# Kernel tuning notes

Hardware: AMD Instinct MI355X
Metric: run time of the kernel (lower is better)

The kernel has to match this reference:

```python
import jax, jax.numpy as jnp
import numpy as np

N, F_IN, H = 8192, 256, 64


def setup_inputs() -> dict:
    key = jax.random.key(0)
    ks = jax.random.split(key, 5)
    seq1 = jax.random.normal(ks[0], (1, N, F_IN), jnp.float32)
    seq2 = jax.random.normal(ks[1], (1, N, F_IN), jnp.float32)
    # dense (row-stochastic-ish) adjacency, batch dim 1 as in DGI usage
    adj = jax.random.uniform(ks[2], (1, N, N), jnp.float32) / np.float32(N)
    msk = jnp.ones((1, N), jnp.float32)
    # GCN params: Linear(in_ft, out_ft, bias=False) weight [H, F_IN], bias [H], PReLU alpha
    fc_w = jax.random.normal(ks[3], (H, F_IN), jnp.float32) / np.float32(np.sqrt(F_IN))
    gcn_bias = jnp.zeros((H,), jnp.float32)
    prelu_alpha = jnp.array(0.25, jnp.float32)
    # Discriminator: Bilinear(H, H, 1) -> weight [H, H], bias scalar
    disc_w = jax.random.normal(ks[4], (H, H), jnp.float32) / np.float32(np.sqrt(H))
    disc_b = jnp.zeros((1,), jnp.float32)
    return {"seq1": seq1, "seq2": seq2, "adj": adj, "msk": msk,
            "fc_w": fc_w, "gcn_bias": gcn_bias, "prelu_alpha": prelu_alpha,
            "disc_w": disc_w, "disc_b": disc_b}


def _gcn(seq, adj, fc_w, bias, alpha):
    fts = jnp.einsum('bnf,hf->bnh', seq, fc_w)          # linear, no bias
    out = jnp.einsum('bnm,bmh->bnh', adj, fts) + bias   # dense aggregation + bias
    return jnp.where(out > 0, out, alpha * out)          # PReLU


def reference(seq1, seq2, adj, msk, fc_w, gcn_bias, prelu_alpha, disc_w, disc_b):
    h1 = _gcn(seq1, adj, fc_w, gcn_bias, prelu_alpha)    # [1, N, H]
    # AvgReadout with mask: sum(seq*msk,1)/sum(msk)
    c = jnp.sum(h1 * msk[..., None], axis=1) / jnp.sum(msk)  # [1, H]
    c = jax.nn.sigmoid(c)
    h2 = _gcn(seq2, adj, fc_w, gcn_bias, prelu_alpha)    # [1, N, H]
    # Bilinear discriminator: sc[b,n] = h[b,n,:] @ W @ c[b,:] + b
    wc = jnp.einsum('hk,bk->bh', disc_w, c)              # [1, H]
    sc1 = jnp.einsum('bnh,bh->bn', h1, wc) + disc_b[0]   # [1, N]
    sc2 = jnp.einsum('bnh,bh->bn', h2, wc) + disc_b[0]   # [1, N]
    return jnp.concatenate([sc1, sc2], axis=1)           # [1, 2N]
```

## Files before the change

kernel.cpp:

```cpp
#include <hip/hip_runtime.h>
#include <cstdint>
#include <cstddef>

#define NN 8192
#define FIN 256
#define HH 64
#define SPLIT 16
#define KLEN (NN / SPLIT)

typedef float vf4 __attribute__((ext_vector_type(4)));
typedef short vbf8 __attribute__((ext_vector_type(8)));

__device__ inline unsigned pk_trunc(float lo, float hi) {
  return __builtin_amdgcn_perm(__float_as_uint(hi), __float_as_uint(lo), 0x07060302u);
}
__device__ inline unsigned short bf_rne(float x) {
  unsigned u = __float_as_uint(x);
  return (unsigned short)((u + 0x7FFFu + ((u >> 16) & 1u)) >> 16);
}
__device__ inline float bf_to_f(unsigned short s) {
  return __uint_as_float(((unsigned)s) << 16);
}

union FragU { unsigned u[4]; unsigned short s[8]; vbf8 v; };

__device__ inline vbf8 frag_trunc(vf4 a, vf4 b) {
  FragU t;
  t.u[0] = pk_trunc(a[0], a[1]);
  t.u[1] = pk_trunc(a[2], a[3]);
  t.u[2] = pk_trunc(b[0], b[1]);
  t.u[3] = pk_trunc(b[2], b[3]);
  return t.v;
}
__device__ inline vbf8 frag_rne(vf4 a, vf4 b) {
  FragU t;
  t.s[0] = bf_rne(a[0]); t.s[1] = bf_rne(a[1]); t.s[2] = bf_rne(a[2]); t.s[3] = bf_rne(a[3]);
  t.s[4] = bf_rne(b[0]); t.s[5] = bf_rne(b[1]); t.s[6] = bf_rne(b[2]); t.s[7] = bf_rne(b[3]);
  return t.v;
}

__device__ inline void gl_lds16(const void* g, void* l) {
  __builtin_amdgcn_global_load_lds(
      (const __attribute__((address_space(1))) void*)g,
      (__attribute__((address_space(3))) void*)l, 16, 0, 0);
}

__global__ __launch_bounds__(256) void k1_fts(
    const float* __restrict__ seq1, const float* __restrict__ seq2,
    const float* __restrict__ fcw, unsigned short* __restrict__ Bt,
    float* __restrict__ csum) {
  const int bx = blockIdx.x;
  const int s = bx & 1, mb = bx >> 1;
  const int wave = threadIdx.x >> 6, lane = threadIdx.x & 63;
  const int r = lane & 15, q = lane >> 4;
  const int m0 = mb * 64 + wave * 16;
  if (bx == 0 && threadIdx.x < 64) csum[threadIdx.x] = 0.f;
  const float* seq = s ? seq2 : seq1;
  const float* ap = seq + (size_t)(m0 + r) * FIN + q * 8;
  const float* bp = fcw + (size_t)r * FIN + q * 8;
  vf4 acc[4] = {};
#pragma unroll
  for (int kk = 0; kk < FIN; kk += 32) {
    vf4 a0 = *(const vf4*)ap;
    vf4 a1 = *(const vf4*)(ap + 4);
    vbf8 af = frag_rne(a0, a1);
#pragma unroll
    for (int f = 0; f < 4; ++f) {
      vf4 b0 = *(const vf4*)(bp + (size_t)f * 16 * FIN);
      vf4 b1 = *(const vf4*)(bp + (size_t)f * 16 * FIN + 4);
      vbf8 bfr = frag_rne(b0, b1);
      acc[f] = __builtin_amdgcn_mfma_f32_16x16x32_bf16(af, bfr, acc[f], 0, 0, 0);
    }
    ap += 32; bp += 32;
  }
#pragma unroll
  for (int f = 0; f < 4; ++f) {
    short4 v;
    v.x = (short)bf_rne(acc[f][0]);
    v.y = (short)bf_rne(acc[f][1]);
    v.z = (short)bf_rne(acc[f][2]);
    v.w = (short)bf_rne(acc[f][3]);
    unsigned short* dst = Bt + (size_t)(64 * s + 16 * f + r) * NN + m0 + q * 4;
    *(short4*)dst = v;
  }
}

__global__ __launch_bounds__(512, 4) void k2_agg(
    const float* __restrict__ adj, const unsigned short* __restrict__ Bt,
    unsigned short* __restrict__ Cpart) {
  constexpr int CHUNKS = KLEN / 128;
  __shared__ unsigned short lds[2][16384];
  const int bx = blockIdx.x;
  const int slice = bx & (SPLIT - 1), mb = bx / SPLIT;
  const int wave = threadIdx.x >> 6, lane = threadIdx.x & 63;
  const int r = lane & 15, q = lane >> 4;
  const int m0 = mb * 256 + wave * 32;
  const int k0 = slice * KLEN;

  auto stage = [&](int ch, int b) {
#pragma unroll
    for (int j = 0; j < 4; ++j) {
      const int g = j * 512 + wave * 64 + lane;
      const int r_ = g & 15, q_ = (g >> 4) & 3, f_ = (g >> 6) & 7, kk_ = g >> 9;
      const unsigned short* src =
          Bt + (size_t)(f_ * 16 + r_) * NN + k0 + ch * 128 + kk_ * 32 + q_ * 8;
      gl_lds16(src, &lds[b][(size_t)(j * 512 + wave * 64) * 8]);
    }
  };

  vf4 acc0[8] = {}, acc1[8] = {};
  const float* a_base0 = adj + (size_t)(m0 + r) * NN + k0 + q * 8;
  const float* a_base1 = a_base0 + (size_t)16 * NN;

  stage(0, 0);
#pragma unroll 1
  for (int ch = 0; ch < CHUNKS; ++ch) {
    __syncthreads();
    if (ch + 1 < CHUNKS) stage(ch + 1, (ch + 1) & 1);
    const int b = ch & 1;
#pragma unroll
    for (int kk = 0; kk < 4; ++kk) {
      const int kc = ch * 128 + kk * 32;
      vf4 a00 = __builtin_nontemporal_load((const vf4*)(a_base0 + kc));
      vf4 a01 = __builtin_nontemporal_load((const vf4*)(a_base0 + kc) + 1);
      vf4 a10 = __builtin_nontemporal_load((const vf4*)(a_base1 + kc));
      vf4 a11 = __builtin_nontemporal_load((const vf4*)(a_base1 + kc) + 1);
      vbf8 af0 = frag_trunc(a00, a01);
      vbf8 af1 = frag_trunc(a10, a11);
#pragma unroll
      for (int f = 0; f < 8; ++f) {
        vbf8 bfr = *(const vbf8*)&lds[b][(size_t)(kk * 512 + f * 64 + lane) * 8];
        acc0[f] = __builtin_amdgcn_mfma_f32_16x16x32_bf16(af0, bfr, acc0[f], 0, 0, 0);
        acc1[f] = __builtin_amdgcn_mfma_f32_16x16x32_bf16(af1, bfr, acc1[f], 0, 0, 0);
      }
    }
  }

#pragma unroll
  for (int f = 0; f < 8; ++f) {
    short4 v0, v1;
    v0.x = (short)bf_rne(acc0[f][0]); v0.y = (short)bf_rne(acc0[f][1]);
    v0.z = (short)bf_rne(acc0[f][2]); v0.w = (short)bf_rne(acc0[f][3]);
    v1.x = (short)bf_rne(acc1[f][0]); v1.y = (short)bf_rne(acc1[f][1]);
    v1.z = (short)bf_rne(acc1[f][2]); v1.w = (short)bf_rne(acc1[f][3]);
    unsigned short* d0 = Cpart + ((size_t)slice * 128 + f * 16 + r) * NN + m0 + q * 4;
    *(short4*)d0 = v0;
    *(short4*)(d0 + 16) = v1;
  }
}

__global__ __launch_bounds__(256) void k3a(
    const unsigned short* __restrict__ Cpart, const float* __restrict__ bias,
    const float* __restrict__ alpha_p, const float* __restrict__ msk,
    unsigned short* __restrict__ H, float* __restrict__ csum) {
  const int n = blockIdx.x >> 2, chunk = blockIdx.x & 3;
  const int t = threadIdx.x;
  const int m0 = chunk * 2048 + t * 8;
  const float alpha = alpha_p[0], b = bias[n & 63];
  float v[8] = {};
#pragma unroll
  for (int s = 0; s < SPLIT; ++s) {
    vbf8 c = *(const vbf8*)(Cpart + ((size_t)s * 128 + n) * NN + m0);
#pragma unroll
    for (int j = 0; j < 8; ++j) v[j] += bf_to_f((unsigned short)c[j]);
  }
  FragU hout;
  float acc = 0.f;
#pragma unroll
  for (int j = 0; j < 8; ++j) {
    float x = v[j] + b;
    x = x > 0.f ? x : alpha * x;
    hout.s[j] = bf_rne(x);
    acc += x * msk[m0 + j];
  }
  *(vbf8*)(H + (size_t)n * NN + m0) = hout.v;
  if (n < 64) {
    __shared__ float red[256];
    red[t] = acc;
    __syncthreads();
    for (int off = 128; off > 32; off >>= 1) {
      if (t < off) red[t] += red[t + off];
      __syncthreads();
    }
    if (t < 32) {
      float x = red[t] + red[t + 32];
#pragma unroll
      for (int off = 16; off > 0; off >>= 1) x += __shfl_down(x, off, 64);
      if (t == 0) atomicAdd(&csum[n], x);
    }
  }
}

__global__ __launch_bounds__(256) void k3b(
    const float* __restrict__ msk, const float* __restrict__ csum,
    const float* __restrict__ discw, float* __restrict__ wc) {
  const int t = threadIdx.x;
  __shared__ float red[256];
  __shared__ float c_sh[64];
  float ms = 0.f;
  for (int i = 0; i < 32; ++i) ms += msk[t + 256 * i];
  red[t] = ms;
  __syncthreads();
  for (int off = 128; off > 0; off >>= 1) {
    if (t < off) red[t] += red[t + off];
    __syncthreads();
  }
  if (t < 64) c_sh[t] = 1.f / (1.f + __expf(-csum[t] / red[0]));
  __syncthreads();
  if (t < 64) {
    float w = 0.f;
#pragma unroll
    for (int k = 0; k < 64; ++k) w += discw[t * 64 + k] * c_sh[k];
    wc[t] = w;
  }
}

__global__ __launch_bounds__(256) void k4_sc(
    const unsigned short* __restrict__ H, const float* __restrict__ wc,
    const float* __restrict__ discb, float* __restrict__ out) {
  const int t = threadIdx.x, lane = t & 63, w = t >> 6;
  const int m = blockIdx.x * 64 + lane;
  float s = 0.f;
#pragma unroll
  for (int i = 0; i < 32; ++i) {
    const int n = w * 32 + i;
    s += bf_to_f(H[(size_t)n * NN + m]) * wc[n & 63];
  }
  __shared__ float red[4][64];
  red[w][lane] = s;
  __syncthreads();
  if (t < 128) {
    const int half = t >> 6, mm = t & 63;
    out[(size_t)half * NN + blockIdx.x * 64 + mm] =
        red[half * 2][mm] + red[half * 2 + 1][mm] + discb[0];
  }
}

extern "C" void kernel_launch(void* const* d_in, const int* in_sizes, int n_in,
                              void* d_out, int out_size, void* d_ws, size_t ws_size,
                              hipStream_t stream) {
  const float* seq1  = (const float*)d_in[0];
  const float* seq2  = (const float*)d_in[1];
  const float* adj   = (const float*)d_in[2];
  const float* msk   = (const float*)d_in[3];
  const float* fcw   = (const float*)d_in[4];
  const float* bias  = (const float*)d_in[5];
  const float* alpha = (const float*)d_in[6];
  const float* discw = (const float*)d_in[7];
  const float* discb = (const float*)d_in[8];
  float* out = (float*)d_out;
  char* ws = (char*)d_ws;

  unsigned short* Bt    = (unsigned short*)ws;
  unsigned short* Cpart = (unsigned short*)(ws + (size_t)(2 << 20));
  unsigned short* H     = (unsigned short*)(ws + (size_t)(34 << 20));
  float* csum           = (float*)(ws + (size_t)(36 << 20));
  float* wc             = csum + 64;

  hipLaunchKernelGGL(k1_fts, dim3(256), dim3(256), 0, stream, seq1, seq2, fcw, Bt, csum);
  hipLaunchKernelGGL(k2_agg, dim3(32 * SPLIT), dim3(512), 0, stream, adj, Bt, Cpart);
  hipLaunchKernelGGL(k3a, dim3(512), dim3(256), 0, stream, Cpart, bias, alpha, msk, H, csum);
  hipLaunchKernelGGL(k3b, dim3(1), dim3(256), 0, stream, msk, csum, discw, wc);
  hipLaunchKernelGGL(k4_sc, dim3(128), dim3(256), 0, stream, H, wc, discb, out);
}
```

Measured before the change: 412.9 us.

## Software-pipeline adjacency loads in aggregation and fold discriminator prep into scoring kernel

In the aggregation kernel, the adjacency fragments for the next k-step are now prefetched into registers while the current step's MFMAs run. The block barrier is replaced by an explicit vmcnt wait plus s_barrier with sched_barriers, so outstanding global loads no longer force a full drain. Separately, the single-block k3b kernel is removed and its mask sum, sigmoid and W·c work is recomputed redundantly in every k4_sc block, saving one launch. This adds register pressure, relies on hand-counted vmcnt values being correct, and repeats a small amount of work per block.

Measured after the change: 426.7 us. 1.03x slower.

```diff
diff --git a/kernel.cpp b/kernel.cpp
--- a/kernel.cpp
+++ b/kernel.cpp
@@ -109,31 +109,45 @@
   };
 
   vf4 acc0[8] = {}, acc1[8] = {};
-  const float* a_base0 = adj + (size_t)(m0 + r) * NN + k0 + q * 8;
-  const float* a_base1 = a_base0 + (size_t)16 * NN;
+  const float* a0p = adj + (size_t)(m0 + r) * NN + k0 + q * 8;
+  const float* a1p = a0p + (size_t)16 * NN;
 
   stage(0, 0);
+  vf4 pa0 = __builtin_nontemporal_load((const vf4*)a0p);
+  vf4 pa1 = __builtin_nontemporal_load((const vf4*)a0p + 1);
+  vf4 pa2 = __builtin_nontemporal_load((const vf4*)a1p);
+  vf4 pa3 = __builtin_nontemporal_load((const vf4*)a1p + 1);
+
 #pragma unroll 1
   for (int ch = 0; ch < CHUNKS; ++ch) {
-    __syncthreads();
-    if (ch + 1 < CHUNKS) stage(ch + 1, (ch + 1) & 1);
     const int b = ch & 1;
+    asm volatile("s_waitcnt vmcnt(4)" ::: "memory");
+    __builtin_amdgcn_s_barrier();
+    __builtin_amdgcn_sched_barrier(0);
+    if (ch + 1 < CHUNKS) stage(ch + 1, b ^ 1);
+    __builtin_amdgcn_sched_barrier(0);
 #pragma unroll
     for (int kk = 0; kk < 4; ++kk) {
-      const int kc = ch * 128 + kk * 32;
-      vf4 a00 = __builtin_nontemporal_load((const vf4*)(a_base0 + kc));
-      vf4 a01 = __builtin_nontemporal_load((const vf4*)(a_base0 + kc) + 1);
-      vf4 a10 = __builtin_nontemporal_load((const vf4*)(a_base1 + kc));
-      vf4 a11 = __builtin_nontemporal_load((const vf4*)(a_base1 + kc) + 1);
-      vbf8 af0 = frag_trunc(a00, a01);
-      vbf8 af1 = frag_trunc(a10, a11);
+      const bool more = (kk < 3) || (ch + 1 < CHUNKS);
+      const int nc = (kk + 1) * 32;
+      vf4 na0, na1, na2, na3;
+      if (more) {
+        na0 = __builtin_nontemporal_load((const vf4*)(a0p + nc));
+        na1 = __builtin_nontemporal_load((const vf4*)(a0p + nc) + 1);
+        na2 = __builtin_nontemporal_load((const vf4*)(a1p + nc));
+        na3 = __builtin_nontemporal_load((const vf4*)(a1p + nc) + 1);
+      }
+      vbf8 af0 = frag_trunc(pa0, pa1);
+      vbf8 af1 = frag_trunc(pa2, pa3);
 #pragma unroll
       for (int f = 0; f < 8; ++f) {
         vbf8 bfr = *(const vbf8*)&lds[b][(size_t)(kk * 512 + f * 64 + lane) * 8];
         acc0[f] = __builtin_amdgcn_mfma_f32_16x16x32_bf16(af0, bfr, acc0[f], 0, 0, 0);
         acc1[f] = __builtin_amdgcn_mfma_f32_16x16x32_bf16(af1, bfr, acc1[f], 0, 0, 0);
       }
-    }
+      if (more) { pa0 = na0; pa1 = na1; pa2 = na2; pa3 = na3; }
+    }
+    a0p += 128; a1p += 128;
   }
 
 #pragma unroll
@@ -191,40 +205,40 @@
   }
 }
 
-__global__ __launch_bounds__(256) void k3b(
-    const float* __restrict__ msk, const float* __restrict__ csum,
-    const float* __restrict__ discw, float* __restrict__ wc) {
-  const int t = threadIdx.x;
-  __shared__ float red[256];
-  __shared__ float c_sh[64];
-  float ms = 0.f;
-  for (int i = 0; i < 32; ++i) ms += msk[t + 256 * i];
-  red[t] = ms;
-  __syncthreads();
-  for (int off = 128; off > 0; off >>= 1) {
-    if (t < off) red[t] += red[t + off];
-    __syncthreads();
-  }
-  if (t < 64) c_sh[t] = 1.f / (1.f + __expf(-csum[t] / red[0]));
-  __syncthreads();
-  if (t < 64) {
-    float w = 0.f;
-#pragma unroll
-    for (int k = 0; k < 64; ++k) w += discw[t * 64 + k] * c_sh[k];
-    wc[t] = w;
-  }
-}
-
 __global__ __launch_bounds__(256) void k4_sc(
-    const unsigned short* __restrict__ H, const float* __restrict__ wc,
+    const unsigned short* __restrict__ H, const float* __restrict__ msk,
+    const float* __restrict__ csum, const float* __restrict__ discw,
     const float* __restrict__ discb, float* __restrict__ out) {
   const int t = threadIdx.x, lane = t & 63, w = t >> 6;
+  __shared__ float red2[256];
+  __shared__ float c_sh[64];
+  __shared__ float wc_sh[64];
+  float ms = 0.f;
+#pragma unroll
+  for (int i = 0; i < 32; ++i) ms += msk[t + 256 * i];
+  red2[t] = ms;
+  __syncthreads();
+  for (int off = 128; off > 0; off >>= 1) {
+    if (t < off) red2[t] += red2[t + off];
+    __syncthreads();
+  }
+  const float msum = red2[0];
+  if (t < 64) c_sh[t] = 1.f / (1.f + __expf(-csum[t] / msum));
+  __syncthreads();
+  if (t < 64) {
+    float wv = 0.f;
+#pragma unroll
+    for (int k = 0; k < 64; ++k) wv += discw[t * 64 + k] * c_sh[k];
+    wc_sh[t] = wv;
+  }
+  __syncthreads();
+
   const int m = blockIdx.x * 64 + lane;
   float s = 0.f;
 #pragma unroll
   for (int i = 0; i < 32; ++i) {
     const int n = w * 32 + i;
-    s += bf_to_f(H[(size_t)n * NN + m]) * wc[n & 63];
+    s += bf_to_f(H[(size_t)n * NN + m]) * wc_sh[n & 63];
   }
   __shared__ float red[4][64];
   red[w][lane] = s;
@@ -255,11 +269,9 @@
   unsigned short* Cpart = (unsigned short*)(ws + (size_t)(2 << 20));
   unsigned short* H     = (unsigned short*)(ws + (size_t)(34 << 20));
   float* csum           = (float*)(ws + (size_t)(36 << 20));
-  float* wc             = csum + 64;
 
   hipLaunchKernelGGL(k1_fts, dim3(256), dim3(256), 0, stream, seq1, seq2, fcw, Bt, csum);
   hipLaunchKernelGGL(k2_agg, dim3(32 * SPLIT), dim3(512), 0, stream, adj, Bt, Cpart);
   hipLaunchKernelGGL(k3a, dim3(512), dim3(256), 0, stream, Cpart, bias, alpha, msk, H, csum);
-  hipLaunchKernelGGL(k3b, dim3(1), dim3(256), 0, stream, msk, csum, discw, wc);
-  hipLaunchKernelGGL(k4_sc, dim3(128), dim3(256), 0, stream, H, wc, discb, out);
-}
+  hipLaunchKernelGGL(k4_sc, dim3(128), dim3(256), 0, stream, H, msk, csum, discw, discb, out);
+}
```
